# Kernel optimization log

Hardware: AMD Instinct MI355X
Metric: run time of the kernel (lower is better)

Reference implementation:

```python
import jax, jax.numpy as jnp
import numpy as np

N = 20000          # nodes (== virtual nodes, forced by scatter dim_size + residuals)
E = 240000         # edges
H = 256            # hidden_dim
SD = 128           # scalar_dim (mult of 0e in "128x0e+64x1o+32x2e")
FEAT = 128 + 64 * 3 + 32 * 5   # 480 = target_irreps dim
C = 4              # vn_channel


def _lin(key, din, dout):
    k1, k2 = jax.random.split(key)
    s = 1.0 / np.sqrt(din)
    w = jax.random.uniform(k1, (din, dout), jnp.float32, -s, s)
    b = jax.random.uniform(k2, (dout,), jnp.float32, -s, s)
    return w, b


def _mlp(x, w1, b1, w2, b2):
    # BaseMLP: Linear -> SiLU -> Linear (no norm, no residual, no last act)
    return jax.nn.silu(x @ w1 + b1) @ w2 + b2


def setup_inputs() -> dict:
    key = jax.random.key(0)
    ks = jax.random.split(key, 12)
    inp = {
        "node_feat": jax.random.normal(ks[0], (N, FEAT), jnp.float32),
        "node_pos": jax.random.normal(ks[1], (N, 3), jnp.float32),
        "vn_feat": jax.random.normal(ks[2], (N, H), jnp.float32),
        "vn_pos": jax.random.normal(ks[3], (N, 3 * C), jnp.float32),
        "edge_index": jax.random.randint(ks[4], (2, E), 0, N),
        "w_scalar": jax.random.normal(ks[5], (SD, SD), jnp.float32),  # e3nn o3.Linear 0e->0e path
    }
    mlps = {"cm": (SD + H + C * C, H), "vr": (H, C), "rv": (H, C * C),
            "ft": (H, H), "f2t": (H, SD), "vf": (H, H)}
    i = 6
    for name, (din, dout) in mlps.items():
        k1, k2 = jax.random.split(ks[i]); i += 1
        inp[name + "_w1"], inp[name + "_b1"] = _lin(k1, din, H)
        inp[name + "_w2"], inp[name + "_b2"] = _lin(k2, H, dout)
    return inp


def reference(node_feat, node_pos, vn_feat, vn_pos, edge_index, w_scalar,
              cm_w1, cm_b1, cm_w2, cm_b2, vr_w1, vr_b1, vr_w2, vr_b2,
              rv_w1, rv_b1, rv_w2, rv_b2, ft_w1, ft_b1, ft_w2, ft_b2,
              f2t_w1, f2t_b1, f2t_w2, f2t_b2, vf_w1, vf_b1, vf_w2, vf_b2):
    n = node_feat.shape[0]
    row, col = edge_index[0], edge_index[1]

    # e3nn o3.Linear(target_irreps -> SDx0e): single 0e->0e path, 1/sqrt(fan_in)
    nfs = (node_feat[:, :SD] @ w_scalar) * (1.0 / np.sqrt(SD))

    # per-edge relative positions between node pos (tiled to C channels) and vn pos
    d = (jnp.tile(node_pos[row], (1, C)) - vn_pos[col]).reshape(-1, C, 3)  # [E,C,3]

    # normalized gram matrix of the C difference vectors
    ip = jnp.einsum('ecj,ekj->eck', d, d).reshape(-1, C * C)
    ip = ip / jnp.maximum(jnp.linalg.norm(ip, axis=-1, keepdims=True), 1e-8)

    dn = d / jnp.maximum(jnp.linalg.norm(d, axis=-1, keepdims=True), 1e-8)  # [E,C,3]

    msg = _mlp(jnp.concatenate([nfs[row], vn_feat[col], ip], axis=1),
               cm_w1, cm_b1, cm_w2, cm_b2)                                   # [E,H]

    w_vr = _mlp(msg, vr_w1, vr_b1, vr_w2, vr_b2)                 # [E,C]
    w_rv = _mlp(msg, rv_w1, rv_b1, rv_w2, rv_b2).reshape(-1, C, C)

    inv = 1.0 / np.sqrt(C)
    # FCTP Cx1o (x) 1x0e -> 1x1o  (x2 == 1): weighted sum of the C vectors
    vr_upd = inv * jnp.einsum('ec,ecj->ej', w_vr, dn)            # [E,3]
    # FCTP Cx1o (x) 1x0e -> Cx1o on -dn
    rv_upd = inv * jnp.einsum('ecu,ecj->euj', w_rv, -dn).reshape(-1, 3 * C)  # [E,3C]

    cnt = jnp.maximum(jax.ops.segment_sum(jnp.ones((row.shape[0],), msg.dtype), row, n), 1.0)[:, None]
    agg_feat = jax.ops.segment_sum(msg, row, n) / cnt            # scatter_mean by row
    agg_vr = jax.ops.segment_sum(vr_upd, row, n) / cnt
    agg_rv = jax.ops.segment_sum(rv_upd, row, n) / cnt

    ds = _mlp(_mlp(agg_feat, ft_w1, ft_b1, ft_w2, ft_b2), f2t_w1, f2t_b1, f2t_w2, f2t_b2)
    node_feat_out = node_feat.at[:, :SD].add(ds)  # delta only hits the scalar (0e) block
    node_pos_out = node_pos + agg_vr
    vn_feat_out = vn_feat + _mlp(agg_feat, vf_w1, vf_b1, vf_w2, vf_b2)
    vn_pos_out = vn_pos + agg_rv
    return node_feat_out, node_pos_out, vn_feat_out, vn_pos_out
```

## Files before the change

kernel.cpp:

```cpp
#include <hip/hip_runtime.h>
#include <hip/hip_bf16.h>
#include <math.h>


#define FEAT 480
#define HDIM 256
#define SDIM 128
#define MSTR 264

#define OW1   0
#define OW2   106496
#define OVR1  172032
#define ORV1  237568
#define OVR2  303104
#define ORV2  307200
#define OFT1  311296
#define OFT2  376832
#define OF2T1 442368
#define OF2T2 507904
#define OVF1  540672
#define OVF2  606208
#define OWTOT 671744

typedef __attribute__((ext_vector_type(8))) short bf16x8;
typedef __attribute__((ext_vector_type(4))) float f32x4;

__device__ __forceinline__ float silu_f(float x) {
    return x / (1.0f + __expf(-x));
}
__device__ __forceinline__ ushort f2b(float v) {
    __hip_bfloat16 h = __float2bfloat16(v);
    return *(ushort*)&h;
}
__device__ __forceinline__ float b2f(ushort u) {
    union { unsigned int i; float f; } c;
    c.i = ((unsigned int)u) << 16;
    return c.f;
}

#define KLOOP2(SRC, WP)                                                        \
    {                                                                          \
        _Pragma("unroll")                                                      \
        for (int mt = 0; mt < 4; ++mt)                                         \
            _Pragma("unroll")                                                  \
            for (int nt = 0; nt < 2; ++nt) acc[mt][nt] = (f32x4)0.f;           \
        _Pragma("unroll")                                                      \
        for (int ks = 0; ks < 8; ++ks) {                                       \
            bf16x8 a_[4];                                                      \
            _Pragma("unroll")                                                  \
            for (int mt = 0; mt < 4; ++mt)                                     \
                a_[mt] = *(const bf16x8*)&(SRC)[(mt * 16 + lr) * MSTR + ks * 32 + lk * 8]; \
            _Pragma("unroll")                                                  \
            for (int nt = 0; nt < 2; ++nt) {                                   \
                const bf16x8 b = *(const bf16x8*)&(WP)[(size_t)(((wv * 2 + nt) * 8 + ks) * 512) + lane * 8]; \
                _Pragma("unroll")                                              \
                for (int mt = 0; mt < 4; ++mt)                                 \
                    acc[mt][nt] = __builtin_amdgcn_mfma_f32_16x16x32_bf16(a_[mt], b, acc[mt][nt], 0, 0, 0); \
            }                                                                  \
        }                                                                      \
    }

#define EPI_SILU2(DST, BIAS)                                                   \
    _Pragma("unroll")                                                          \
    for (int nt = 0; nt < 2; ++nt) {                                           \
        const int col = colBase + nt * 16 + lr;                                \
        const float bb = (BIAS)[col];                                          \
        _Pragma("unroll")                                                      \
        for (int mt = 0; mt < 4; ++mt)                                         \
            _Pragma("unroll")                                                  \
            for (int r = 0; r < 4; ++r) {                                      \
                const int row = mt * 16 + lk * 4 + r;                          \
                (DST)[row * MSTR + col] = f2b(silu_f(acc[mt][nt][r] + bb));    \
            }                                                                  \
    }

#define KLOOP_FR(SRC, WP)                                                      \
    {                                                                          \
        _Pragma("unroll")                                                      \
        for (int mt = 0; mt < 2; ++mt)                                         \
            _Pragma("unroll")                                                  \
            for (int nt = 0; nt < 4; ++nt) accn[mt][nt] = (f32x4)0.f;          \
        _Pragma("unroll")                                                      \
        for (int ks = 0; ks < 8; ++ks) {                                       \
            const bf16x8 a0 = *(const bf16x8*)&(SRC)[lr * MSTR + ks * 32 + lk * 8];        \
            const bf16x8 a1 = *(const bf16x8*)&(SRC)[(lr + 16) * MSTR + ks * 32 + lk * 8]; \
            _Pragma("unroll")                                                  \
            for (int nt = 0; nt < 4; ++nt) {                                   \
                const bf16x8 b = *(const bf16x8*)&(WP)[(size_t)(((wv * 4 + nt) * 8 + ks) * 512) + lane * 8]; \
                accn[0][nt] = __builtin_amdgcn_mfma_f32_16x16x32_bf16(a0, b, accn[0][nt], 0, 0, 0); \
                accn[1][nt] = __builtin_amdgcn_mfma_f32_16x16x32_bf16(a1, b, accn[1][nt], 0, 0, 0); \
            }                                                                  \
        }                                                                      \
    }

#define EPI_SILUN(DST, BIAS)                                                   \
    _Pragma("unroll")                                                          \
    for (int nt = 0; nt < 4; ++nt) {                                           \
        const int col = colBase + nt * 16 + lr;                                \
        const float bb = (BIAS)[col];                                          \
        _Pragma("unroll")                                                      \
        for (int mt = 0; mt < 2; ++mt)                                         \
            _Pragma("unroll")                                                  \
            for (int r = 0; r < 4; ++r) {                                      \
                const int row = mt * 16 + lk * 4 + r;                          \
                (DST)[row * MSTR + col] = f2b(silu_f(accn[mt][nt][r] + bb));   \
            }                                                                  \
    }

__global__ __launch_bounds__(256) void k_count(
    const int* __restrict__ eidx, int* __restrict__ cnt_i, int E)
{
    const int e = blockIdx.x * 256 + threadIdx.x;
    if (e < E) atomicAdd(&cnt_i[eidx[e]], 1);
}

__global__ __launch_bounds__(1024) void k_scan(
    const int* __restrict__ cnt_i, int* __restrict__ rowstart,
    float* __restrict__ cntf, int Nn)
{
    __shared__ int sh[1024];
    __shared__ int carry_s;
    const int t = threadIdx.x;
    if (t == 0) carry_s = 0;
    __syncthreads();
    const int nch = (Nn + 1023) / 1024;
    for (int ch = 0; ch < nch; ++ch) {
        const int i = ch * 1024 + t;
        const int v = (i < Nn) ? cnt_i[i] : 0;
        sh[t] = v;
        __syncthreads();
        for (int off = 1; off < 1024; off <<= 1) {
            const int add = (t >= off) ? sh[t - off] : 0;
            __syncthreads();
            sh[t] += add;
            __syncthreads();
        }
        const int incl = sh[t];
        const int carry = carry_s;
        if (i < Nn) {
            rowstart[i + 1] = carry + incl;
            cntf[i] = fmaxf((float)v, 1.0f);
        }
        __syncthreads();
        if (t == 1023) carry_s = carry + incl;
        __syncthreads();
    }
    if (t == 0) rowstart[0] = 0;
}

__global__ __launch_bounds__(256) void k_place(
    const int* __restrict__ eidx, const int* __restrict__ rowstart,
    int* __restrict__ cursor, int* __restrict__ elist, int E)
{
    const int e = blockIdx.x * 256 + threadIdx.x;
    if (e < E) {
        const int r = eidx[e];
        const int p = atomicAdd(&cursor[r], 1);
        elist[rowstart[r] + p] = e;
    }
}

__global__ __launch_bounds__(256) void k_wprep(
    const float* __restrict__ w1, const float* __restrict__ w2,
    const float* __restrict__ vrw1, const float* __restrict__ rvw1,
    const float* __restrict__ vrw2, const float* __restrict__ rvw2,
    const float* __restrict__ ftw1, const float* __restrict__ ftw2,
    const float* __restrict__ f2tw1, const float* __restrict__ f2tw2,
    const float* __restrict__ vfw1, const float* __restrict__ vfw2,
    ushort* __restrict__ wb)
{
    const int idx = blockIdx.x * 256 + threadIdx.x;
    if (idx >= OWTOT) return;
    ushort v;
    if (idx < OW2) {
        const int o = idx, f = o >> 9, l = (o >> 3) & 63, e = o & 7;
        const int nt = f / 13, ks = f % 13;
        const int col = nt * 16 + (l & 15);
        const int k = ks * 32 + ((l >> 4) << 3) + e;
        v = (k < 400) ? f2b(w1[(size_t)k * 256 + col]) : (ushort)0;
    } else if (idx < OVR1) {
        const int o = idx - OW2, f = o >> 9, l = (o >> 3) & 63, e = o & 7;
        const int col = (f >> 3) * 16 + (l & 15);
        const int k = (f & 7) * 32 + ((l >> 4) << 3) + e;
        v = f2b(w2[(size_t)k * 256 + col]);
    } else if (idx < ORV1) {
        const int o = idx - OVR1, f = o >> 9, l = (o >> 3) & 63, e = o & 7;
        const int col = (f >> 3) * 16 + (l & 15);
        const int k = (f & 7) * 32 + ((l >> 4) << 3) + e;
        v = f2b(vrw1[(size_t)k * 256 + col]);
    } else if (idx < OVR2) {
        const int o = idx - ORV1, f = o >> 9, l = (o >> 3) & 63, e = o & 7;
        const int col = (f >> 3) * 16 + (l & 15);
        const int k = (f & 7) * 32 + ((l >> 4) << 3) + e;
        v = f2b(rvw1[(size_t)k * 256 + col]);
    } else if (idx < ORV2) {
        const int o = idx - OVR2, f = o >> 9, l = (o >> 3) & 63, e = o & 7;
        const int col = l & 15;
        const int k = f * 32 + ((l >> 4) << 3) + e;
        v = (col < 4) ? f2b(vrw2[(size_t)k * 4 + col]) : (ushort)0;
    } else if (idx < OFT1) {
        const int o = idx - ORV2, f = o >> 9, l = (o >> 3) & 63, e = o & 7;
        const int col = l & 15;
        const int k = f * 32 + ((l >> 4) << 3) + e;
        v = f2b(rvw2[(size_t)k * 16 + col]);
    } else if (idx < OFT2) {
        const int o = idx - OFT1, f = o >> 9, l = (o >> 3) & 63, e = o & 7;
        const int col = (f >> 3) * 16 + (l & 15);
        const int k = (f & 7) * 32 + ((l >> 4) << 3) + e;
        v = f2b(ftw1[(size_t)k * 256 + col]);
    } else if (idx < OF2T1) {
        const int o = idx - OFT2, f = o >> 9, l = (o >> 3) & 63, e = o & 7;
        const int col = (f >> 3) * 16 + (l & 15);
        const int k = (f & 7) * 32 + ((l >> 4) << 3) + e;
        v = f2b(ftw2[(size_t)k * 256 + col]);
    } else if (idx < OF2T2) {
        const int o = idx - OF2T1, f = o >> 9, l = (o >> 3) & 63, e = o & 7;
        const int col = (f >> 3) * 16 + (l & 15);
        const int k = (f & 7) * 32 + ((l >> 4) << 3) + e;
        v = f2b(f2tw1[(size_t)k * 256 + col]);
    } else if (idx < OVF1) {
        const int o = idx - OF2T2, f = o >> 9, l = (o >> 3) & 63, e = o & 7;
        const int col = (f >> 3) * 16 + (l & 15);
        const int k = (f & 7) * 32 + ((l >> 4) << 3) + e;
        v = f2b(f2tw2[(size_t)k * 128 + col]);
    } else if (idx < OVF2) {
        const int o = idx - OVF1, f = o >> 9, l = (o >> 3) & 63, e = o & 7;
        const int col = (f >> 3) * 16 + (l & 15);
        const int k = (f & 7) * 32 + ((l >> 4) << 3) + e;
        v = f2b(vfw1[(size_t)k * 256 + col]);
    } else {
        const int o = idx - OVF2, f = o >> 9, l = (o >> 3) & 63, e = o & 7;
        const int col = (f >> 3) * 16 + (l & 15);
        const int k = (f & 7) * 32 + ((l >> 4) << 3) + e;
        v = f2b(vfw2[(size_t)k * 256 + col]);
    }
    wb[idx] = v;
}

__global__ __launch_bounds__(256) void k_vnb(
    const float* __restrict__ vn_feat, ushort* __restrict__ vnb, int total4)
{
    const int i = blockIdx.x * 256 + threadIdx.x;
    if (i >= total4) return;
    const float4 v = *(const float4*)&vn_feat[(size_t)i * 4];
    ushort4 o;
    o.x = f2b(v.x); o.y = f2b(v.y); o.z = f2b(v.z); o.w = f2b(v.w);
    *(ushort4*)&vnb[(size_t)i * 4] = o;
}

__global__ __launch_bounds__(256) void k_nfs(
    const float* __restrict__ node_feat, const float* __restrict__ w_scalar,
    ushort* __restrict__ nfsb)
{
    __shared__ float At[32][20];
    __shared__ float Wt[16][128];
    const int t  = threadIdx.x;
    const int m0 = blockIdx.x * 32;
    const int c4 = (t & 31) * 4;
    const int rg = t >> 5;
    float acc[4][4] = {};
    for (int k0 = 0; k0 < 128; k0 += 16) {
        if (t < 128) {
            const int r = t >> 2, kk = (t & 3) * 4;
            *(float4*)&At[r][kk] =
                *(const float4*)&node_feat[(size_t)(m0 + r) * FEAT + k0 + kk];
        }
        #pragma unroll
        for (int i = 0; i < 2; ++i) {
            const int p  = t + i * 256;
            const int wr = p >> 5, wc = (p & 31) * 4;
            *(float4*)&Wt[wr][wc] =
                *(const float4*)&w_scalar[(size_t)(k0 + wr) * SDIM + wc];
        }
        __syncthreads();
        #pragma unroll
        for (int kk = 0; kk < 16; ++kk) {
            const float4 w = *(const float4*)&Wt[kk][c4];
            #pragma unroll
            for (int j = 0; j < 4; ++j) {
                const float a = At[rg * 4 + j][kk];
                acc[j][0] = fmaf(a, w.x, acc[j][0]);
                acc[j][1] = fmaf(a, w.y, acc[j][1]);
                acc[j][2] = fmaf(a, w.z, acc[j][2]);
                acc[j][3] = fmaf(a, w.w, acc[j][3]);
            }
        }
        __syncthreads();
    }
    const float s = 0.08838834764831845f;
    #pragma unroll
    for (int j = 0; j < 4; ++j) {
        ushort4 o;
        o.x = f2b(acc[j][0] * s); o.y = f2b(acc[j][1] * s);
        o.z = f2b(acc[j][2] * s); o.w = f2b(acc[j][3] * s);
        *(ushort4*)&nfsb[(size_t)(m0 + rg * 4 + j) * SDIM + c4] = o;
    }
}

__global__ __launch_bounds__(512, 4) void k_edge(
    const ushort* __restrict__ nfsb, const ushort* __restrict__ vnb,
    const float* __restrict__ node_pos, const float* __restrict__ vn_pos,
    const int* __restrict__ eidx, const int* __restrict__ elist,
    const ushort* __restrict__ wb,
    const float* __restrict__ b1, const float* __restrict__ b2,
    const float* __restrict__ vrb1, const float* __restrict__ vrb2,
    const float* __restrict__ rvb1, const float* __restrict__ rvb2,
    float* __restrict__ agg_feat, float* __restrict__ agg_vr,
    float* __restrict__ agg_rv, int E)
{
    __shared__ ushort Mg[64 * MSTR];
    __shared__ ushort Hd[64 * MSTR];
    __shared__ ushort ipB[64 * 16];
    __shared__ float dnS[64][12];
    __shared__ float wvrS[64][4];
    __shared__ float wrvS[64][16];
    __shared__ int rowi[64], coli[64];

    const int t  = threadIdx.x;
    const int e0 = blockIdx.x * 64;
    const int wv = t >> 6;
    const int lane = t & 63;
    const int lr = lane & 15;
    const int lk = lane >> 4;
    const int colBase = wv * 32;

    if (t < 64) {
        const int e = elist[e0 + t];
        const int r = eidx[e];
        const int c = eidx[E + e];
        rowi[t] = r; coli[t] = c;
        const float px = node_pos[r * 3 + 0];
        const float py = node_pos[r * 3 + 1];
        const float pz = node_pos[r * 3 + 2];
        float d[4][3];
        #pragma unroll
        for (int ch = 0; ch < 4; ++ch) {
            d[ch][0] = px - vn_pos[(size_t)c * 12 + ch * 3 + 0];
            d[ch][1] = py - vn_pos[(size_t)c * 12 + ch * 3 + 1];
            d[ch][2] = pz - vn_pos[(size_t)c * 12 + ch * 3 + 2];
        }
        float ss = 0.f, ipv[16];
        #pragma unroll
        for (int ci = 0; ci < 4; ++ci)
            #pragma unroll
            for (int ck = 0; ck < 4; ++ck) {
                const float v = d[ci][0]*d[ck][0] + d[ci][1]*d[ck][1] + d[ci][2]*d[ck][2];
                ipv[ci * 4 + ck] = v; ss += v * v;
            }
        const float inrm = 1.0f / fmaxf(sqrtf(ss), 1e-8f);
        #pragma unroll
        for (int i = 0; i < 16; ++i) ipB[t * 16 + i] = f2b(ipv[i] * inrm);
        #pragma unroll
        for (int ch = 0; ch < 4; ++ch) {
            const float nn = sqrtf(d[ch][0]*d[ch][0] + d[ch][1]*d[ch][1] + d[ch][2]*d[ch][2]);
            const float s = 1.0f / fmaxf(nn, 1e-8f);
            dnS[t][ch * 3 + 0] = d[ch][0] * s;
            dnS[t][ch * 3 + 1] = d[ch][1] * s;
            dnS[t][ch * 3 + 2] = d[ch][2] * s;
        }
    }
    __syncthreads();

    const ushort* nA[4]; const ushort* vA[4];
    #pragma unroll
    for (int mt = 0; mt < 4; ++mt) {
        nA[mt] = nfsb + (size_t)rowi[mt * 16 + lr] * SDIM + lk * 8;
        vA[mt] = vnb  + (size_t)coli[mt * 16 + lr] * HDIM + lk * 8;
    }
    const ushort* w1t = wb + OW1;

    f32x4 acc[4][2];

    #pragma unroll
    for (int mt = 0; mt < 4; ++mt)
        #pragma unroll
        for (int nt = 0; nt < 2; ++nt) acc[mt][nt] = (f32x4)0.f;
    #pragma unroll
    for (int ks = 0; ks < 13; ++ks) {
        bf16x8 a_[4];
        #pragma unroll
        for (int mt = 0; mt < 4; ++mt) {
            if (ks < 4)       a_[mt] = *(const bf16x8*)(nA[mt] + ks * 32);
            else if (ks < 12) a_[mt] = *(const bf16x8*)(vA[mt] + ks * 32 - 128);
            else if (lk < 2)  a_[mt] = *(const bf16x8*)&ipB[(mt * 16 + lr) * 16 + lk * 8];
            else              a_[mt] = (bf16x8)(short)0;
        }
        #pragma unroll
        for (int nt = 0; nt < 2; ++nt) {
            const bf16x8 b = *(const bf16x8*)&w1t[(size_t)(((wv * 2 + nt) * 13 + ks) * 512) + lane * 8];
            #pragma unroll
            for (int mt = 0; mt < 4; ++mt)
                acc[mt][nt] = __builtin_amdgcn_mfma_f32_16x16x32_bf16(a_[mt], b, acc[mt][nt], 0, 0, 0);
        }
    }
    EPI_SILU2(Hd, b1);
    __syncthreads();

    KLOOP2(Hd, wb + OW2);
    #pragma unroll
    for (int nt = 0; nt < 2; ++nt) {
        const int col = colBase + nt * 16 + lr;
        const float bb = b2[col];
        #pragma unroll
        for (int mt = 0; mt < 4; ++mt)
            #pragma unroll
            for (int r = 0; r < 4; ++r) {
                const int row = mt * 16 + lk * 4 + r;
                Mg[row * MSTR + col] = f2b(acc[mt][nt][r] + bb);
            }
    }
    __syncthreads();

    {
        const int col = t & 255;
        const int r0 = (t >> 8) * 32;
        float s = 0.f;
        int prev = rowi[r0];
        for (int r = r0; r < r0 + 32; ++r) {
            const int rr = rowi[r];
            if (rr != prev) {
                atomicAdd(&agg_feat[(size_t)prev * HDIM + col], s);
                s = 0.f; prev = rr;
            }
            s += b2f(Mg[r * MSTR + col]);
        }
        atomicAdd(&agg_feat[(size_t)prev * HDIM + col], s);
    }

    KLOOP2(Mg, wb + OVR1);
    EPI_SILU2(Hd, vrb1);
    __syncthreads();

    if ((wv & 3) == 0) {
        const int rb = (wv >> 2) * 32;
        const ushort* vrw2t = wb + OVR2;
        f32x4 a2[2]; a2[0] = (f32x4)0.f; a2[1] = (f32x4)0.f;
        #pragma unroll
        for (int ks = 0; ks < 8; ++ks) {
            const bf16x8 a0 = *(const bf16x8*)&Hd[(rb + lr) * MSTR + ks * 32 + lk * 8];
            const bf16x8 a1 = *(const bf16x8*)&Hd[(rb + 16 + lr) * MSTR + ks * 32 + lk * 8];
            const bf16x8 b  = *(const bf16x8*)&vrw2t[(size_t)(ks * 512) + lane * 8];
            a2[0] = __builtin_amdgcn_mfma_f32_16x16x32_bf16(a0, b, a2[0], 0, 0, 0);
            a2[1] = __builtin_amdgcn_mfma_f32_16x16x32_bf16(a1, b, a2[1], 0, 0, 0);
        }
        if (lr < 4) {
            const float bb = vrb2[lr];
            #pragma unroll
            for (int mt = 0; mt < 2; ++mt)
                #pragma unroll
                for (int r = 0; r < 4; ++r)
                    wvrS[rb + mt * 16 + lk * 4 + r][lr] = a2[mt][r] + bb;
        }
    }
    __syncthreads();

    KLOOP2(Mg, wb + ORV1);
    EPI_SILU2(Hd, rvb1);
    __syncthreads();

    if ((wv & 3) == 0) {
        const int rb = (wv >> 2) * 32;
        const ushort* rvw2t = wb + ORV2;
        f32x4 a2[2]; a2[0] = (f32x4)0.f; a2[1] = (f32x4)0.f;
        #pragma unroll
        for (int ks = 0; ks < 8; ++ks) {
            const bf16x8 a0 = *(const bf16x8*)&Hd[(rb + lr) * MSTR + ks * 32 + lk * 8];
            const bf16x8 a1 = *(const bf16x8*)&Hd[(rb + 16 + lr) * MSTR + ks * 32 + lk * 8];
            const bf16x8 b  = *(const bf16x8*)&rvw2t[(size_t)(ks * 512) + lane * 8];
            a2[0] = __builtin_amdgcn_mfma_f32_16x16x32_bf16(a0, b, a2[0], 0, 0, 0);
            a2[1] = __builtin_amdgcn_mfma_f32_16x16x32_bf16(a1, b, a2[1], 0, 0, 0);
        }
        const float bb = rvb2[lr];
        #pragma unroll
        for (int mt = 0; mt < 2; ++mt)
            #pragma unroll
            for (int r = 0; r < 4; ++r)
                wrvS[rb + mt * 16 + lk * 4 + r][lr] = a2[mt][r] + bb;
    }
    __syncthreads();

    if (t < 64) {
        float wvv[4], wrr[16], dn[12], ev[15];
        #pragma unroll
        for (int c = 0; c < 4; ++c)  wvv[c] = wvrS[t][c];
        #pragma unroll
        for (int i = 0; i < 16; ++i) wrr[i] = wrvS[t][i];
        #pragma unroll
        for (int i = 0; i < 12; ++i) dn[i]  = dnS[t][i];
        #pragma unroll
        for (int j = 0; j < 3; ++j) {
            float v = 0.f;
            #pragma unroll
            for (int c = 0; c < 4; ++c) v = fmaf(wvv[c], dn[c * 3 + j], v);
            ev[j] = 0.5f * v;
        }
        #pragma unroll
        for (int u = 0; u < 4; ++u)
            #pragma unroll
            for (int j = 0; j < 3; ++j) {
                float v = 0.f;
                #pragma unroll
                for (int c = 0; c < 4; ++c) v = fmaf(wrr[c * 4 + u], dn[c * 3 + j], v);
                ev[3 + u * 3 + j] = -0.5f * v;
            }
        #pragma unroll
        for (int i = 0; i < 15; ++i) wrvS[t][i] = ev[i];
    }
    __syncthreads();

    if ((t & 255) < 15 && t < 512) {
        const int comp = t & 255;
        if (t < 256 || t >= 256) {
            const int r0 = (t >> 8) * 32;
            float s = 0.f;
            int prev = rowi[r0];
            for (int r = r0; r < r0 + 32; ++r) {
                const int rr = rowi[r];
                if (rr != prev) {
                    if (comp < 3) atomicAdd(&agg_vr[(size_t)prev * 3 + comp], s);
                    else          atomicAdd(&agg_rv[(size_t)prev * 12 + (comp - 3)], s);
                    s = 0.f; prev = rr;
                }
                s += wrvS[r][comp];
            }
            if (comp < 3) atomicAdd(&agg_vr[(size_t)prev * 3 + comp], s);
            else          atomicAdd(&agg_rv[(size_t)prev * 12 + (comp - 3)], s);
        }
    }
}

__global__ __launch_bounds__(256, 4) void k_node(
    const float* __restrict__ node_feat, const float* __restrict__ node_pos,
    const float* __restrict__ vn_feat, const float* __restrict__ vn_pos,
    const float* __restrict__ agg_feat, const float* __restrict__ agg_vr,
    const float* __restrict__ agg_rv, const float* __restrict__ cntf,
    const ushort* __restrict__ wb,
    const float* __restrict__ ftb1, const float* __restrict__ ftb2,
    const float* __restrict__ f2tb1, const float* __restrict__ f2tb2,
    const float* __restrict__ vfb1, const float* __restrict__ vfb2,
    float* __restrict__ out, int Nn)
{
    __shared__ ushort Ab[32 * MSTR];
    __shared__ ushort Hd[32 * MSTR];
    __shared__ float rc[32];
    const int t  = threadIdx.x;
    const int n0 = blockIdx.x * 32;
    const int wv = t >> 6;
    const int lane = t & 63;
    const int lr = lane & 15;
    const int lk = lane >> 4;
    const int colBase = wv * 64;

    float* nf_out = out;
    float* np_out = out + (size_t)Nn * FEAT;
    float* vf_out = np_out + (size_t)Nn * 3;
    float* vp_out = vf_out + (size_t)Nn * HDIM;

    if (t < 32) rc[t] = 1.0f / fmaxf(cntf[n0 + t], 1.0f);
    __syncthreads();
    #pragma unroll
    for (int i = 0; i < 8; ++i) {
        const int p = t + i * 256;
        const int r = p >> 6, cc = (p & 63) * 4;
        float4 v = *(const float4*)&agg_feat[(size_t)(n0 + r) * HDIM + cc];
        const float s = rc[r];
        ushort4 o;
        o.x = f2b(v.x * s); o.y = f2b(v.y * s);
        o.z = f2b(v.z * s); o.w = f2b(v.w * s);
        *(ushort4*)&Ab[r * MSTR + cc] = o;
    }
    __syncthreads();

    f32x4 accn[2][4];

    KLOOP_FR(Ab, wb + OVF1);
    EPI_SILUN(Hd, vfb1);
    __syncthreads();
    KLOOP_FR(Hd, wb + OVF2);
    #pragma unroll
    for (int nt = 0; nt < 4; ++nt) {
        const int col = colBase + nt * 16 + lr;
        const float bb = vfb2[col];
        #pragma unroll
        for (int mt = 0; mt < 2; ++mt)
            #pragma unroll
            for (int r = 0; r < 4; ++r) {
                const int row = mt * 16 + lk * 4 + r;
                const size_t o = (size_t)(n0 + row) * HDIM + col;
                vf_out[o] = vn_feat[o] + accn[mt][nt][r] + bb;
            }
    }
    __syncthreads();

    KLOOP_FR(Ab, wb + OFT1);
    EPI_SILUN(Hd, ftb1);
    __syncthreads();
    KLOOP_FR(Hd, wb + OFT2);
    #pragma unroll
    for (int nt = 0; nt < 4; ++nt) {
        const int col = colBase + nt * 16 + lr;
        const float bb = ftb2[col];
        #pragma unroll
        for (int mt = 0; mt < 2; ++mt)
            #pragma unroll
            for (int r = 0; r < 4; ++r) {
                const int row = mt * 16 + lk * 4 + r;
                Ab[row * MSTR + col] = f2b(accn[mt][nt][r] + bb);
            }
    }
    __syncthreads();

    KLOOP_FR(Ab, wb + OF2T1);
    EPI_SILUN(Hd, f2tb1);
    __syncthreads();
    {
        const ushort* w2p = wb + OF2T2;
        f32x4 a2[2][2];
        #pragma unroll
        for (int mt = 0; mt < 2; ++mt)
            #pragma unroll
            for (int nt = 0; nt < 2; ++nt) a2[mt][nt] = (f32x4)0.f;
        #pragma unroll
        for (int ks = 0; ks < 8; ++ks) {
            const int k0 = ks * 32 + lk * 8;
            const bf16x8 a0 = *(const bf16x8*)&Hd[lr * MSTR + k0];
            const bf16x8 a1 = *(const bf16x8*)&Hd[(lr + 16) * MSTR + k0];
            const bf16x8 w0 = *(const bf16x8*)&w2p[(size_t)(((wv * 2 + 0) * 8 + ks) * 512) + lane * 8];
            const bf16x8 w1v = *(const bf16x8*)&w2p[(size_t)(((wv * 2 + 1) * 8 + ks) * 512) + lane * 8];
            a2[0][0] = __builtin_amdgcn_mfma_f32_16x16x32_bf16(a0, w0, a2[0][0], 0, 0, 0);
            a2[1][0] = __builtin_amdgcn_mfma_f32_16x16x32_bf16(a1, w0, a2[1][0], 0, 0, 0);
            a2[0][1] = __builtin_amdgcn_mfma_f32_16x16x32_bf16(a0, w1v, a2[0][1], 0, 0, 0);
            a2[1][1] = __builtin_amdgcn_mfma_f32_16x16x32_bf16(a1, w1v, a2[1][1], 0, 0, 0);
        }
        #pragma unroll
        for (int nt = 0; nt < 2; ++nt) {
            const int col = wv * 32 + nt * 16 + lr;
            const float bb = f2tb2[col];
            #pragma unroll
            for (int mt = 0; mt < 2; ++mt)
                #pragma unroll
                for (int r = 0; r < 4; ++r) {
                    const int row = mt * 16 + lk * 4 + r;
                    const size_t o = (size_t)(n0 + row) * FEAT + col;
                    nf_out[o] = node_feat[o] + a2[mt][nt][r] + bb;
                }
        }
    }

    for (int p = t; p < 32 * 88; p += 256) {
        const int r = p / 88;
        const int cc = 128 + (p % 88) * 4;
        const size_t o = (size_t)(n0 + r) * FEAT + cc;
        *(float4*)&nf_out[o] = *(const float4*)&node_feat[o];
    }
    if (t < 32) {
        const int n = n0 + t;
        const float s = rc[t];
        #pragma unroll
        for (int j = 0; j < 3; ++j)
            np_out[(size_t)n * 3 + j] = node_pos[(size_t)n * 3 + j] + agg_vr[(size_t)n * 3 + j] * s;
        #pragma unroll
        for (int j = 0; j < 12; ++j)
            vp_out[(size_t)n * 12 + j] = vn_pos[(size_t)n * 12 + j] + agg_rv[(size_t)n * 12 + j] * s;
    }
}

extern "C" void kernel_launch(void* const* d_in, const int* in_sizes, int n_in,
                              void* d_out, int out_size, void* d_ws, size_t ws_size,
                              hipStream_t stream)
{
    (void)n_in; (void)out_size; (void)ws_size;
    const float* node_feat = (const float*)d_in[0];
    const float* node_pos  = (const float*)d_in[1];
    const float* vn_feat   = (const float*)d_in[2];
    const float* vn_pos    = (const float*)d_in[3];
    const int*   eidx      = (const int*)d_in[4];
    const float* w_scalar  = (const float*)d_in[5];
    const float* cm_w1  = (const float*)d_in[6];
    const float* cm_b1  = (const float*)d_in[7];
    const float* cm_w2  = (const float*)d_in[8];
    const float* cm_b2  = (const float*)d_in[9];
    const float* vr_w1  = (const float*)d_in[10];
    const float* vr_b1  = (const float*)d_in[11];
    const float* vr_w2  = (const float*)d_in[12];
    const float* vr_b2  = (const float*)d_in[13];
    const float* rv_w1  = (const float*)d_in[14];
    const float* rv_b1  = (const float*)d_in[15];
    const float* rv_w2  = (const float*)d_in[16];
    const float* rv_b2  = (const float*)d_in[17];
    const float* ft_w1  = (const float*)d_in[18];
    const float* ft_b1  = (const float*)d_in[19];
    const float* ft_w2  = (const float*)d_in[20];
    const float* ft_b2  = (const float*)d_in[21];
    const float* f2t_w1 = (const float*)d_in[22];
    const float* f2t_b1 = (const float*)d_in[23];
    const float* f2t_w2 = (const float*)d_in[24];
    const float* f2t_b2 = (const float*)d_in[25];
    const float* vf_w1  = (const float*)d_in[26];
    const float* vf_b1  = (const float*)d_in[27];
    const float* vf_w2  = (const float*)d_in[28];
    const float* vf_b2  = (const float*)d_in[29];

    const int Nn = in_sizes[0] / FEAT;
    const int E  = in_sizes[4] / 2;

    float* ws       = (float*)d_ws;
    float* agg_feat = ws;
    float* agg_vr   = agg_feat + (size_t)Nn * HDIM;
    float* agg_rv   = agg_vr   + (size_t)Nn * 3;
    float* cntf     = agg_rv   + (size_t)Nn * 12;
    int*   cnt_i    = (int*)(cntf + Nn);
    int*   cursor   = cnt_i + Nn;
    int*   rowstart = cursor + Nn;
    int*   elist    = rowstart + Nn + 16;
    ushort* nfsb = (ushort*)(elist + E);
    ushort* vnb  = nfsb + (size_t)Nn * SDIM;
    ushort* wb   = vnb  + (size_t)Nn * HDIM;

    const size_t zero_bytes = (size_t)Nn * (HDIM + 3 + 12 + 1 + 2) * sizeof(float);
    hipMemsetAsync(agg_feat, 0, zero_bytes, stream);

    const int eg = (E + 255) / 256;
    k_count<<<eg, 256, 0, stream>>>(eidx, cnt_i, E);
    k_scan<<<1, 1024, 0, stream>>>(cnt_i, rowstart, cntf, Nn);
    k_place<<<eg, 256, 0, stream>>>(eidx, rowstart, cursor, elist, E);
    k_wprep<<<(OWTOT + 255) / 256, 256, 0, stream>>>(
        cm_w1, cm_w2, vr_w1, rv_w1, vr_w2, rv_w2,
        ft_w1, ft_w2, f2t_w1, f2t_w2, vf_w1, vf_w2, wb);
    k_vnb<<<(Nn * 64 + 255) / 256, 256, 0, stream>>>(vn_feat, vnb, Nn * 64);
    k_nfs<<<Nn / 32, 256, 0, stream>>>(node_feat, w_scalar, nfsb);
    k_edge<<<E / 64, 512, 0, stream>>>(nfsb, vnb, node_pos, vn_pos, eidx, elist,
                                       wb, cm_b1, cm_b2, vr_b1, vr_b2, rv_b1, rv_b2,
                                       agg_feat, agg_vr, agg_rv, E);
    k_node<<<Nn / 32, 256, 0, stream>>>(node_feat, node_pos, vn_feat, vn_pos,
                                        agg_feat, agg_vr, agg_rv, cntf, wb,
                                        ft_b1, ft_b2, f2t_b1, f2t_b2, vf_b1, vf_b2,
                                        (float*)d_out, Nn);
}
```

Baseline: 489.2 us.

## Parallelize row-start scan and fuse vr/rv first-layer GEMMs in edge kernel

The single-block serial scan over 20 chunks is replaced by a three-kernel parallel scan: per-block scans, a tiny block-sum scan, and an add-back pass. In the edge kernel, the vr and rv hidden-layer GEMMs now share one K loop over the message tile, writing vr into Hd and rv into Mg. This lets the two small second-layer GEMMs run concurrently on different waves and removes a pair of barriers. It adds two kernel launches and more accumulator registers per wave, which may reduce occupancy. Mg is overwritten after its last reader, guarded by a barrier placed before the epilogue.

```diff
diff --git a/kernel.cpp b/kernel.cpp
--- a/kernel.cpp
+++ b/kernel.cpp
@@ -114,38 +114,43 @@
     if (e < E) atomicAdd(&cnt_i[eidx[e]], 1);
 }
 
-__global__ __launch_bounds__(1024) void k_scan(
+__global__ __launch_bounds__(1024) void k_scanA(
     const int* __restrict__ cnt_i, int* __restrict__ rowstart,
-    float* __restrict__ cntf, int Nn)
+    float* __restrict__ cntf, int* __restrict__ bsum, int Nn)
 {
     __shared__ int sh[1024];
-    __shared__ int carry_s;
     const int t = threadIdx.x;
-    if (t == 0) carry_s = 0;
-    __syncthreads();
-    const int nch = (Nn + 1023) / 1024;
-    for (int ch = 0; ch < nch; ++ch) {
-        const int i = ch * 1024 + t;
-        const int v = (i < Nn) ? cnt_i[i] : 0;
-        sh[t] = v;
+    const int i = blockIdx.x * 1024 + t;
+    const int v = (i < Nn) ? cnt_i[i] : 0;
+    sh[t] = v;
+    __syncthreads();
+    for (int off = 1; off < 1024; off <<= 1) {
+        const int add = (t >= off) ? sh[t - off] : 0;
         __syncthreads();
-        for (int off = 1; off < 1024; off <<= 1) {
-            const int add = (t >= off) ? sh[t - off] : 0;
-            __syncthreads();
-            sh[t] += add;
-            __syncthreads();
-        }
-        const int incl = sh[t];
-        const int carry = carry_s;
-        if (i < Nn) {
-            rowstart[i + 1] = carry + incl;
-            cntf[i] = fmaxf((float)v, 1.0f);
-        }
+        sh[t] += add;
         __syncthreads();
-        if (t == 1023) carry_s = carry + incl;
-        __syncthreads();
-    }
-    if (t == 0) rowstart[0] = 0;
+    }
+    if (i < Nn) {
+        rowstart[i + 1] = sh[t];
+        cntf[i] = fmaxf((float)v, 1.0f);
+    }
+    if (t == 1023) bsum[blockIdx.x] = sh[t];
+}
+
+__global__ __launch_bounds__(64) void k_scanB(int* __restrict__ bsum, int nb)
+{
+    if (threadIdx.x == 0) {
+        int s = 0;
+        for (int i = 0; i < nb; ++i) { const int v = bsum[i]; bsum[i] = s; s += v; }
+    }
+}
+
+__global__ __launch_bounds__(1024) void k_scanC(
+    int* __restrict__ rowstart, const int* __restrict__ bsum, int Nn)
+{
+    const int i = blockIdx.x * 1024 + threadIdx.x;
+    if (i < Nn) rowstart[i + 1] += bsum[blockIdx.x];
+    if (i == 0) rowstart[0] = 0;
 }
 
 __global__ __launch_bounds__(256) void k_place(
@@ -427,8 +432,46 @@
         atomicAdd(&agg_feat[(size_t)prev * HDIM + col], s);
     }
 
-    KLOOP2(Mg, wb + OVR1);
-    EPI_SILU2(Hd, vrb1);
+    {
+        f32x4 accV[4][2], accR[4][2];
+        #pragma unroll
+        for (int mt = 0; mt < 4; ++mt)
+            #pragma unroll
+            for (int nt = 0; nt < 2; ++nt) { accV[mt][nt] = (f32x4)0.f; accR[mt][nt] = (f32x4)0.f; }
+        #pragma unroll
+        for (int ks = 0; ks < 8; ++ks) {
+            bf16x8 a_[4];
+            #pragma unroll
+            for (int mt = 0; mt < 4; ++mt)
+                a_[mt] = *(const bf16x8*)&Mg[(mt * 16 + lr) * MSTR + ks * 32 + lk * 8];
+            #pragma unroll
+            for (int nt = 0; nt < 2; ++nt) {
+                const bf16x8 bv = *(const bf16x8*)&wb[OVR1 + (size_t)(((wv * 2 + nt) * 8 + ks) * 512) + lane * 8];
+                #pragma unroll
+                for (int mt = 0; mt < 4; ++mt)
+                    accV[mt][nt] = __builtin_amdgcn_mfma_f32_16x16x32_bf16(a_[mt], bv, accV[mt][nt], 0, 0, 0);
+                const bf16x8 br = *(const bf16x8*)&wb[ORV1 + (size_t)(((wv * 2 + nt) * 8 + ks) * 512) + lane * 8];
+                #pragma unroll
+                for (int mt = 0; mt < 4; ++mt)
+                    accR[mt][nt] = __builtin_amdgcn_mfma_f32_16x16x32_bf16(a_[mt], br, accR[mt][nt], 0, 0, 0);
+            }
+        }
+        __syncthreads();
+        #pragma unroll
+        for (int nt = 0; nt < 2; ++nt) {
+            const int col = colBase + nt * 16 + lr;
+            const float bv = vrb1[col];
+            const float br = rvb1[col];
+            #pragma unroll
+            for (int mt = 0; mt < 4; ++mt)
+                #pragma unroll
+                for (int r = 0; r < 4; ++r) {
+                    const int row = mt * 16 + lk * 4 + r;
+                    Hd[row * MSTR + col] = f2b(silu_f(accV[mt][nt][r] + bv));
+                    Mg[row * MSTR + col] = f2b(silu_f(accR[mt][nt][r] + br));
+                }
+        }
+    }
     __syncthreads();
 
     if ((wv & 3) == 0) {
@@ -451,21 +494,14 @@
                 for (int r = 0; r < 4; ++r)
                     wvrS[rb + mt * 16 + lk * 4 + r][lr] = a2[mt][r] + bb;
         }
-    }
-    __syncthreads();
-
-    KLOOP2(Mg, wb + ORV1);
-    EPI_SILU2(Hd, rvb1);
-    __syncthreads();
-
-    if ((wv & 3) == 0) {
+    } else if ((wv & 3) == 1) {
         const int rb = (wv >> 2) * 32;
         const ushort* rvw2t = wb + ORV2;
         f32x4 a2[2]; a2[0] = (f32x4)0.f; a2[1] = (f32x4)0.f;
         #pragma unroll
         for (int ks = 0; ks < 8; ++ks) {
-            const bf16x8 a0 = *(const bf16x8*)&Hd[(rb + lr) * MSTR + ks * 32 + lk * 8];
-            const bf16x8 a1 = *(const bf16x8*)&Hd[(rb + 16 + lr) * MSTR + ks * 32 + lk * 8];
+            const bf16x8 a0 = *(const bf16x8*)&Mg[(rb + lr) * MSTR + ks * 32 + lk * 8];
+            const bf16x8 a1 = *(const bf16x8*)&Mg[(rb + 16 + lr) * MSTR + ks * 32 + lk * 8];
             const bf16x8 b  = *(const bf16x8*)&rvw2t[(size_t)(ks * 512) + lane * 8];
             a2[0] = __builtin_amdgcn_mfma_f32_16x16x32_bf16(a0, b, a2[0], 0, 0, 0);
             a2[1] = __builtin_amdgcn_mfma_f32_16x16x32_bf16(a1, b, a2[1], 0, 0, 0);
@@ -508,24 +544,22 @@
     }
     __syncthreads();
 
-    if ((t & 255) < 15 && t < 512) {
+    if ((t & 255) < 15) {
         const int comp = t & 255;
-        if (t < 256 || t >= 256) {
-            const int r0 = (t >> 8) * 32;
-            float s = 0.f;
-            int prev = rowi[r0];
-            for (int r = r0; r < r0 + 32; ++r) {
-                const int rr = rowi[r];
-                if (rr != prev) {
-                    if (comp < 3) atomicAdd(&agg_vr[(size_t)prev * 3 + comp], s);
-                    else          atomicAdd(&agg_rv[(size_t)prev * 12 + (comp - 3)], s);
-                    s = 0.f; prev = rr;
-                }
-                s += wrvS[r][comp];
-            }
-            if (comp < 3) atomicAdd(&agg_vr[(size_t)prev * 3 + comp], s);
-            else          atomicAdd(&agg_rv[(size_t)prev * 12 + (comp - 3)], s);
-        }
+        const int r0 = (t >> 8) * 32;
+        float s = 0.f;
+        int prev = rowi[r0];
+        for (int r = r0; r < r0 + 32; ++r) {
+            const int rr = rowi[r];
+            if (rr != prev) {
+                if (comp < 3) atomicAdd(&agg_vr[(size_t)prev * 3 + comp], s);
+                else          atomicAdd(&agg_rv[(size_t)prev * 12 + (comp - 3)], s);
+                s = 0.f; prev = rr;
+            }
+            s += wrvS[r][comp];
+        }
+        if (comp < 3) atomicAdd(&agg_vr[(size_t)prev * 3 + comp], s);
+        else          atomicAdd(&agg_rv[(size_t)prev * 12 + (comp - 3)], s);
     }
 }
 
@@ -712,7 +746,8 @@
     int*   cnt_i    = (int*)(cntf + Nn);
     int*   cursor   = cnt_i + Nn;
     int*   rowstart = cursor + Nn;
-    int*   elist    = rowstart + Nn + 16;
+    int*   bsum     = rowstart + Nn + 8;
+    int*   elist    = bsum + 64;
     ushort* nfsb = (ushort*)(elist + E);
     ushort* vnb  = nfsb + (size_t)Nn * SDIM;
     ushort* wb   = vnb  + (size_t)Nn * HDIM;
@@ -721,8 +756,11 @@
     hipMemsetAsync(agg_feat, 0, zero_bytes, stream);
 
     const int eg = (E + 255) / 256;
+    const int sb = (Nn + 1023) / 1024;
     k_count<<<eg, 256, 0, stream>>>(eidx, cnt_i, E);
-    k_scan<<<1, 1024, 0, stream>>>(cnt_i, rowstart, cntf, Nn);
+    k_scanA<<<sb, 1024, 0, stream>>>(cnt_i, rowstart, cntf, bsum, Nn);
+    k_scanB<<<1, 64, 0, stream>>>(bsum, sb);
+    k_scanC<<<sb, 1024, 0, stream>>>(rowstart, bsum, Nn);
     k_place<<<eg, 256, 0, stream>>>(eidx, rowstart, cursor, elist, E);
     k_wprep<<<(OWTOT + 255) / 256, 256, 0, stream>>>(
         cm_w1, cm_w2, vr_w1, rv_w1, vr_w2, rv_w2,
```

Result: faster. 467.7 us (-4.4%).
